# Optimization experiments

Hardware: AMD Instinct MI355X
Metric: run time of the kernel (lower is better)

## Reference

```python
import jax, jax.numpy as jnp
import numpy as np

N, H, T, E, L = 50000, 128, 4, 150000, 2
LAYER_TIMESTEPS = [3, 3]


def _gru_cell(x_in, h, Wih, Whh, bih, bhh):
    # PyTorch GRUCell semantics. Wih: [3H, in], Whh: [3H, H]
    gx = x_in @ Wih.T + bih
    gh = h @ Whh.T + bhh
    xr, xz, xn = jnp.split(gx, 3, axis=-1)
    hr, hz, hn = jnp.split(gh, 3, axis=-1)
    r = jax.nn.sigmoid(xr + hr)
    z = jax.nn.sigmoid(xz + hz)
    n = jnp.tanh(xn + r * hn)
    return (1.0 - z) * n + z * h


def setup_inputs() -> dict:
    key = jax.random.key(0)
    ks = jax.random.split(key, 16)
    s = 0.02
    inp = {
        'x': jax.random.normal(ks[0], (N, H), dtype=jnp.float32),
        'edges': jax.random.randint(ks[1], (T, E, 2), 0, N, dtype=jnp.int32),
        # per-layer, per-edge-type message linears (Linear: y = x W^T + b)
        'msg_W': jax.random.normal(ks[2], (L, T, H, H), dtype=jnp.float32) * s,
        'msg_b': jax.random.normal(ks[3], (L, T, H), dtype=jnp.float32) * s,
        # GRU layer 0: input dim H
        'gru0_Wih': jax.random.normal(ks[4], (3 * H, H), dtype=jnp.float32) * s,
        'gru0_Whh': jax.random.normal(ks[5], (3 * H, H), dtype=jnp.float32) * s,
        'gru0_bih': jax.random.normal(ks[6], (3 * H,), dtype=jnp.float32) * s,
        'gru0_bhh': jax.random.normal(ks[7], (3 * H,), dtype=jnp.float32) * s,
        # GRU layer 1: residual from layer 0 => input dim 2H
        'gru1_Wih': jax.random.normal(ks[8], (3 * H, 2 * H), dtype=jnp.float32) * s,
        'gru1_Whh': jax.random.normal(ks[9], (3 * H, H), dtype=jnp.float32) * s,
        'gru1_bih': jax.random.normal(ks[10], (3 * H,), dtype=jnp.float32) * s,
        'gru1_bhh': jax.random.normal(ks[11], (3 * H,), dtype=jnp.float32) * s,
    }
    return inp


def _incoming_messages(h, edges, W_l, b_l):
    # gather source states per edge type: [T, E, H]
    src = edges[:, :, 0]
    tgt = edges[:, :, 1]
    h_src = h[src]
    # per-edge-type linear: y = x W^T + b
    msgs = jnp.einsum('teh,tfh->tef', h_src, W_l) + b_l[:, None, :]
    # scatter-add messages onto target nodes (== dense one-hot matmul in original)
    return jax.ops.segment_sum(msgs.reshape(T * E, H), tgt.reshape(T * E), num_segments=N)


def reference(x, edges, msg_W, msg_b, gru0_Wih, gru0_Whh, gru0_bih, gru0_bhh,
              gru1_Wih, gru1_Whh, gru1_bih, gru1_bhh):
    # layer 0
    h = x
    for _ in range(LAYER_TIMESTEPS[0]):
        inc = _incoming_messages(h, edges, msg_W[0], msg_b[0])
        h = _gru_cell(inc, h, gru0_Wih, gru0_Whh, gru0_bih, gru0_bhh)
    h0_out = h
    # layer 1 with residual from initial node representation (layer index 0)
    h = h0_out
    for _ in range(LAYER_TIMESTEPS[1]):
        inc = _incoming_messages(h, edges, msg_W[1], msg_b[1])
        inp = jnp.concatenate([x, inc], axis=-1)  # residual states come first
        h = _gru_cell(inp, h, gru1_Wih, gru1_Whh, gru1_bih, gru1_bhh)
    return h
```

## Files before the change

kernel.cpp:

```cpp
#include <hip/hip_runtime.h>
#include <cstddef>

#define NN 50000
#define HH 128
#define TT 4
#define EE 150000

typedef __attribute__((ext_vector_type(8))) short bfrag8;
typedef __attribute__((ext_vector_type(4))) float f32x4;
typedef __attribute__((ext_vector_type(8))) unsigned short u16x8;

__device__ __forceinline__ float sigm(float v) { return 1.0f / (1.0f + __expf(-v)); }

__device__ __forceinline__ unsigned short f2b(float f) {
    unsigned int u = __float_as_uint(f);
    u += 0x7fffu + ((u >> 16) & 1u);
    return (unsigned short)(u >> 16);
}
__device__ __forceinline__ float b2f(unsigned short s) {
    return __uint_as_float(((unsigned int)s) << 16);
}

__device__ __forceinline__ void gload_lds16(const void* gp, void* lp) {
    __builtin_amdgcn_global_load_lds(
        (const __attribute__((address_space(1))) unsigned int*)gp,
        (__attribute__((address_space(3))) unsigned int*)lp, 16, 0, 0);
}

__device__ __forceinline__ void stage_w(const unsigned short* __restrict__ W, int K,
                                        int rowoff, int g8, unsigned short* ldsbase,
                                        int tid, int w, int lane) {
    #pragma unroll
    for (int i = 0; i < 2; ++i) {
        const int r = i * 64 + w * 8 + (lane >> 3);
        const int sc = g8 * 8 + ((lane & 7) ^ (r & 7));
        gload_lds16(W + (size_t)(rowoff + r) * K + sc * 8, ldsbase + (i * 512 + tid) * 8);
    }
}

__global__ __launch_bounds__(256)
void place_bucket(const int* __restrict__ edges, int* __restrict__ degT,
                  unsigned short* __restrict__ rowsT) {
    int eg = blockIdx.x * 256 + threadIdx.x;
    if (eg >= TT * EE) return;
    int t = eg / EE;
    int src = edges[eg * 2];
    int tgt = edges[eg * 2 + 1];
    int p = atomicAdd(&degT[t * NN + tgt], 1);
    if (p < 32) rowsT[((size_t)t * NN + tgt) * 32 + p] = (unsigned short)src;
}

__global__ __launch_bounds__(256)
void setup_convert(const float* __restrict__ msg_W,
                   const float* __restrict__ W0ih, const float* __restrict__ W0hh,
                   const float* __restrict__ W1ih, const float* __restrict__ W1hh,
                   const float* __restrict__ b0ih, const float* __restrict__ b0hh,
                   const float* __restrict__ b1ih, const float* __restrict__ b1hh,
                   const float* __restrict__ x, const int* __restrict__ degT,
                   unsigned int* __restrict__ degP,
                   unsigned short* __restrict__ wb, float* __restrict__ biasP,
                   unsigned short* __restrict__ xb, unsigned short* __restrict__ hbA,
                   unsigned short* __restrict__ hbB, float* __restrict__ out) {
    int i = blockIdx.x * 256 + threadIdx.x;
    if (i < NN) {
        unsigned int v0 = degT[i];            if (v0 > 32) v0 = 32;
        unsigned int v1 = degT[NN + i];       if (v1 > 32) v1 = 32;
        unsigned int v2 = degT[2 * NN + i];   if (v2 > 32) v2 = 32;
        unsigned int v3 = degT[3 * NN + i];   if (v3 > 32) v3 = 32;
        degP[i] = v0 | (v1 << 8) | (v2 << 16) | (v3 << 24);
        return;
    }
    i -= NN;
    if (i < 131072) {
        int l = i >> 16, r = i & 65535;
        int f = r >> 9, k = r & 511, t = k >> 7, h = k & 127;
        wb[i] = f2b(msg_W[l * 65536 + t * 16384 + f * 128 + h]);
        return;
    }
    i -= 131072;
    if (i < 65536) {
        int p = i >> 8, k = i & 255;
        int g = p >> 7, gc = p & 127;
        int f = g * 128 + gc;
        float v = (k < 128) ? W0ih[f * 128 + k] : W0hh[f * 128 + (k - 128)];
        wb[131072 + i] = f2b(v);
        return;
    }
    i -= 65536;
    if (i < 98304) {
        int p = i / 384, k = i - p * 384;
        int g = p >> 7, gc = p & 127;
        int f = g * 128 + gc;
        float v = (k < 256) ? W1ih[f * 256 + k] : W1hh[f * 128 + (k - 256)];
        wb[196608 + i] = f2b(v);
        return;
    }
    i -= 98304;
    if (i < 16384) {
        int gc = i >> 7, k = i & 127;
        wb[294912 + i] = f2b(W0ih[(256 + gc) * 128 + k]);
        return;
    }
    i -= 16384;
    if (i < 32768) {
        int gc = i >> 8, k = i & 255;
        wb[311296 + i] = f2b(W1ih[(256 + gc) * 256 + k]);
        return;
    }
    i -= 32768;
    if (i < 16384) {
        int gc = i >> 7, k = i & 127;
        wb[344064 + i] = f2b(W0hh[(256 + gc) * 128 + k]);
        return;
    }
    i -= 16384;
    if (i < 16384) {
        int gc = i >> 7, k = i & 127;
        wb[360448 + i] = f2b(W1hh[(256 + gc) * 128 + k]);
        return;
    }
    i -= 16384;
    if (i < 1024) {
        int l = i >> 9, r = i & 511;
        const float* bi = l ? b1ih : b0ih;
        const float* bh = l ? b1hh : b0hh;
        float v;
        if (r < 256) {
            int g = r >> 7, gc = r & 127;
            v = bi[g * 128 + gc] + bh[g * 128 + gc];
        } else if (r < 384) {
            v = bi[256 + (r - 256)];
        } else {
            v = bh[256 + (r - 384)];
        }
        biasP[i] = v;
        return;
    }
    i -= 1024;
    if (i < NN * HH) {
        float v = x[i];
        unsigned short b = f2b(v);
        xb[i] = b;
        hbA[i] = b;
        out[i] = v;
        return;
    }
    i -= NN * HH;
    if (i < 128) {
        hbA[(size_t)NN * 128 + i] = 0;
        hbB[(size_t)NN * 128 + i] = 0;
    }
}

template<int L>
__global__ __launch_bounds__(512, 4)
void step_kernel(const unsigned int* __restrict__ degP,
                 const unsigned short* __restrict__ rowsT,
                 const unsigned short* __restrict__ hb,
                 const unsigned short* __restrict__ xb,
                 const unsigned short* __restrict__ Bm,
                 const float* __restrict__ mb,
                 const unsigned short* __restrict__ Wrz,
                 const unsigned short* __restrict__ Wxn,
                 const unsigned short* __restrict__ Whn,
                 const float* __restrict__ bias,
                 const float* __restrict__ hcur,
                 float* __restrict__ hnext,
                 unsigned short* __restrict__ hbn) {
    constexpr int Kih = L ? 256 : 128;
    constexpr int KRZ = Kih + 128;
    constexpr int NRZ = KRZ / 64;
    constexpr int NXN = Kih / 64;
    constexpr int NT  = 2 * NRZ + NXN + 2;
    __shared__ unsigned short lds[32768];
    constexpr int OFF_S = 0, OFF_BMA = 16384, OFF_BMB = 24576;
    constexpr int OFF_X = 0;
    constexpr int OFF_I = L ? 8192 : 0;
    constexpr int OFF_H = L ? 16384 : 8192;
    constexpr int OFF_WA = L ? 24576 : 16384;
    constexpr int OFF_WB = 24576;

    const int tid = threadIdx.x;
    const int lane = tid & 63;
    const int w = tid >> 6;
    const int ln15 = lane & 15;
    const int quad = lane >> 4;
    const int swz = ln15 & 7;
    const int mbase = blockIdx.x * 64;

    auto do_gather = [&](int ta) {
        const int tsub = lane >> 5;
        const int t = ta + tsub;
        const int jh = (lane >> 4) & 1;
        const int cl = lane & 15;
        const int cc = cl * 8;
        int node0 = mbase + w * 8 + jh * 4;
        if (node0 > NN - 4) node0 = NN - 4;
        const uint4 dp4 = *(const uint4*)&degP[node0];
        const int tsh = t * 8;
        const size_t rbase = ((size_t)t * NN + node0) * 32;
        const u16x8 ix0 = *(const u16x8*)&rowsT[rbase];
        const u16x8 ix1 = *(const u16x8*)&rowsT[rbase + 32];
        const u16x8 ix2 = *(const u16x8*)&rowsT[rbase + 64];
        const u16x8 ix3 = *(const u16x8*)&rowsT[rbase + 96];
        #pragma unroll
        for (int jj = 0; jj < 4; ++jj) {
            const unsigned int dpw = (jj == 0) ? dp4.x : (jj == 1) ? dp4.y : (jj == 2) ? dp4.z : dp4.w;
            const int m = (int)((dpw >> tsh) & 255u);
            const u16x8 ix = (jj == 0) ? ix0 : (jj == 1) ? ix1 : (jj == 2) ? ix2 : ix3;
            float a[8] = {0.f, 0.f, 0.f, 0.f, 0.f, 0.f, 0.f, 0.f};
            #pragma unroll
            for (int q = 0; q < 8; ++q) {
                unsigned int rowi = (unsigned short)ix[q];
                if (q >= m) rowi = NN;
                const u16x8 v = *(const u16x8*)&hb[(size_t)rowi * 128 + cc];
                #pragma unroll
                for (int e = 0; e < 8; ++e) a[e] += b2f((unsigned short)v[e]);
            }
            if (m > 8) {
                const unsigned short* rp = &rowsT[rbase + jj * 32];
                for (int p = 8; p < m; ++p) {
                    const u16x8 v = *(const u16x8*)&hb[(size_t)rp[p] * 128 + cc];
                    #pragma unroll
                    for (int e = 0; e < 8; ++e) a[e] += b2f((unsigned short)v[e]);
                }
            }
            const int lrow = w * 8 + jh * 4 + jj;
            const int kg = tsub * 16 + cl;
            const int pos = (kg & ~7) | ((kg & 7) ^ (lrow & 7));
            u16x8 o;
            #pragma unroll
            for (int e = 0; e < 8; ++e) o[e] = f2b(a[e]);
            *(u16x8*)&lds[OFF_S + lrow * 256 + pos * 8] = o;
        }
    };

    f32x4 ainc[4];
    #pragma unroll
    for (int mt = 0; mt < 4; ++mt) ainc[mt] = (f32x4){0.f, 0.f, 0.f, 0.f};

    stage_w(Bm, 512, 0, 0, &lds[OFF_BMA], tid, w, lane);
    #pragma unroll
    for (int P = 0; P < 2; ++P) {
        do_gather(P * 2);
        __syncthreads();
        #pragma unroll
        for (int tt2 = 0; tt2 < 4; ++tt2) {
            const int tix = P * 4 + tt2;
            if (tix < 7)
                stage_w(Bm, 512, 0, tix + 1,
                        &lds[((tix + 1) & 1) ? OFF_BMB : OFF_BMA], tid, w, lane);
            const int bmoff = (tix & 1) ? OFF_BMB : OFF_BMA;
            #pragma unroll
            for (int kk = 0; kk < 2; ++kk) {
                const int cpos = (kk * 4 + quad) ^ swz;
                bfrag8 aFv[4];
                #pragma unroll
                for (int mt = 0; mt < 4; ++mt)
                    aFv[mt] = *(const bfrag8*)&lds[OFF_S + (mt * 16 + ln15) * 256 + (tt2 * 8 + cpos) * 8];
                const bfrag8 bFv = *(const bfrag8*)&lds[bmoff + ((w * 16 + ln15) * 8 + cpos) * 8];
                #pragma unroll
                for (int mt = 0; mt < 4; ++mt)
                    ainc[mt] = __builtin_amdgcn_mfma_f32_16x16x32_bf16(aFv[mt], bFv, ainc[mt], 0, 0, 0);
            }
            __syncthreads();
        }
    }

    #pragma unroll
    for (int i = 0; i < 2; ++i) {
        const int r0 = i * 32 + w * 4;
        const int row = r0 + (lane >> 4);
        const int pos = lane & 15;
        int grow = mbase + row;
        if (grow > NN - 1) grow = NN - 1;
        const int sc = (pos & 8) | ((pos & 7) ^ (row & 7));
        const size_t off = (size_t)grow * 128 + sc * 8;
        if (L == 1) gload_lds16(xb + off, &lds[OFF_X + r0 * 128]);
        gload_lds16(hb + off, &lds[OFF_H + r0 * 128]);
    }
    stage_w(Wrz, KRZ, 0, 0, &lds[OFF_WA], tid, w, lane);
    {
        const int gc = w * 16 + ln15;
        const float bt0 = mb[gc], bt1 = mb[128 + gc], bt2 = mb[256 + gc], bt3 = mb[384 + gc];
        const int chunk = gc >> 3;
        const int sub = gc & 7;
        #pragma unroll
        for (int mt = 0; mt < 4; ++mt) {
            #pragma unroll
            for (int reg = 0; reg < 4; ++reg) {
                const int lrow = mt * 16 + quad * 4 + reg;
                int row = mbase + lrow;
                if (row > NN - 1) row = NN - 1;
                const unsigned int dp = degP[row];
                const float v = ainc[mt][reg]
                    + (float)(dp & 255u) * bt0 + (float)((dp >> 8) & 255u) * bt1
                    + (float)((dp >> 16) & 255u) * bt2 + (float)((dp >> 24) & 255u) * bt3;
                const int pos = (chunk & 8) | ((chunk & 7) ^ (lrow & 7));
                lds[OFF_I + lrow * 128 + pos * 8 + sub] = f2b(v);
            }
        }
    }
    __syncthreads();

    f32x4 arz0[4], arz1[4], axn[4], ahn[4];
    #pragma unroll
    for (int mt = 0; mt < 4; ++mt) {
        arz0[mt] = (f32x4){0.f, 0.f, 0.f, 0.f};
        arz1[mt] = (f32x4){0.f, 0.f, 0.f, 0.f};
        axn[mt] = (f32x4){0.f, 0.f, 0.f, 0.f};
        ahn[mt] = (f32x4){0.f, 0.f, 0.f, 0.f};
    }

    auto stage_T = [&](int T, int woff) {
        if (L == 0) {
            if (T < 8)       stage_w(Wrz, KRZ, (T >> 2) * 128, T & 3, &lds[woff], tid, w, lane);
            else if (T < 10) stage_w(Wxn, Kih, 0, T - 8, &lds[woff], tid, w, lane);
            else             stage_w(Whn, 128, 0, T - 10, &lds[woff], tid, w, lane);
        } else {
            if (T < 12)      stage_w(Wrz, KRZ, (T / 6) * 128, T % 6, &lds[woff], tid, w, lane);
            else if (T < 16) stage_w(Wxn, Kih, 0, T - 12, &lds[woff], tid, w, lane);
            else             stage_w(Whn, 128, 0, T - 16, &lds[woff], tid, w, lane);
        }
    };
    auto mfma_T = [&](int T, int woff) {
        int abase, ha;
        f32x4* acc;
        if (L == 0) {
            if (T < 8)       { const int hh = T & 3; abase = hh < 2 ? OFF_I : OFF_H; ha = hh & 1; acc = (T >> 2) ? arz1 : arz0; }
            else if (T < 10) { abase = OFF_I; ha = T - 8; acc = axn; }
            else             { abase = OFF_H; ha = T - 10; acc = ahn; }
        } else {
            if (T < 12)      { const int hh = T % 6; abase = hh < 2 ? OFF_X : (hh < 4 ? OFF_I : OFF_H); ha = hh & 1; acc = (T / 6) ? arz1 : arz0; }
            else if (T < 16) { const int hh = T - 12; abase = hh < 2 ? OFF_X : OFF_I; ha = hh & 1; acc = axn; }
            else             { abase = OFF_H; ha = T - 16; acc = ahn; }
        }
        #pragma unroll
        for (int kk = 0; kk < 2; ++kk) {
            const int cpos = (kk * 4 + quad) ^ swz;
            bfrag8 aFv[4];
            #pragma unroll
            for (int mt = 0; mt < 4; ++mt)
                aFv[mt] = *(const bfrag8*)&lds[abase + (mt * 16 + ln15) * 128 + (ha * 8 + cpos) * 8];
            const bfrag8 bFv = *(const bfrag8*)&lds[woff + ((w * 16 + ln15) * 8 + cpos) * 8];
            #pragma unroll
            for (int mt = 0; mt < 4; ++mt)
                acc[mt] = __builtin_amdgcn_mfma_f32_16x16x32_bf16(aFv[mt], bFv, acc[mt], 0, 0, 0);
        }
    };

    if (L == 0) {
        #pragma unroll
        for (int T = 0; T < NT; ++T) {
            if (T + 1 < NT) stage_T(T + 1, ((T + 1) & 1) ? OFF_WB : OFF_WA);
            mfma_T(T, (T & 1) ? OFF_WB : OFF_WA);
            __syncthreads();
        }
    } else {
        #pragma unroll
        for (int T = 0; T < NT; ++T) {
            mfma_T(T, OFF_WB);
            if (T + 1 < NT) {
                __syncthreads();
                stage_T(T + 1, OFF_WB);
                __syncthreads();
            }
        }
    }

    {
        const int gc = w * 16 + ln15;
        const float br = bias[gc];
        const float bz = bias[128 + gc];
        const float bxnv = bias[256 + gc];
        const float bhnv = bias[384 + gc];
        #pragma unroll
        for (int mt = 0; mt < 4; ++mt) {
            #pragma unroll
            for (int reg = 0; reg < 4; ++reg) {
                const int row = mbase + mt * 16 + quad * 4 + reg;
                if (row < NN) {
                    const float r = sigm(arz0[mt][reg] + br);
                    const float z = sigm(arz1[mt][reg] + bz);
                    const float n = tanhf(axn[mt][reg] + bxnv + r * (ahn[mt][reg] + bhnv));
                    const float h = hcur[(size_t)row * 128 + gc];
                    const float o = (1.f - z) * n + z * h;
                    hnext[(size_t)row * 128 + gc] = o;
                    if (hbn) hbn[(size_t)row * 128 + gc] = f2b(o);
                }
            }
        }
    }
}

extern "C" void kernel_launch(void* const* d_in, const int* in_sizes, int n_in,
                              void* d_out, int out_size, void* d_ws, size_t ws_size,
                              hipStream_t stream) {
    (void)in_sizes; (void)n_in; (void)out_size; (void)ws_size;
    const float* x     = (const float*)d_in[0];
    const int*   edges = (const int*)d_in[1];
    const float* msg_W = (const float*)d_in[2];
    const float* msg_b = (const float*)d_in[3];
    const float* W0ih  = (const float*)d_in[4];
    const float* W0hh  = (const float*)d_in[5];
    const float* b0ih  = (const float*)d_in[6];
    const float* b0hh  = (const float*)d_in[7];
    const float* W1ih  = (const float*)d_in[8];
    const float* W1hh  = (const float*)d_in[9];
    const float* b1ih  = (const float*)d_in[10];
    const float* b1hh  = (const float*)d_in[11];
    float* out = (float*)d_out;

    float* ws = (float*)d_ws;
    unsigned short* xb  = (unsigned short*)ws;
    unsigned short* hbA = (unsigned short*)(ws + 3200000);
    unsigned short* hbB = (unsigned short*)(ws + 6400100);
    float* hA           = ws + 9700000;
    unsigned short* wb  = (unsigned short*)(ws + 16200000);
    float* biasP        = ws + 16400000;
    int* degT           = (int*)(ws + 16500000);
    unsigned int* degP  = (unsigned int*)(ws + 16750000);
    unsigned short* rowsT = (unsigned short*)(ws + 16850000);

    unsigned short* Bmsg = wb;
    unsigned short* Wrz0 = wb + 131072;
    unsigned short* Wrz1 = wb + 196608;
    unsigned short* Wxn0 = wb + 294912;
    unsigned short* Wxn1 = wb + 311296;
    unsigned short* Whn0 = wb + 344064;
    unsigned short* Whn1 = wb + 360448;

    hipMemsetAsync(degT, 0, (size_t)NN * 4 * sizeof(int), stream);
    place_bucket<<<(TT * EE + 255) / 256, 256, 0, stream>>>(edges, degT, rowsT);

    setup_convert<<<26672, 256, 0, stream>>>(msg_W, W0ih, W0hh, W1ih, W1hh,
                                             b0ih, b0hh, b1ih, b1hh, x,
                                             degT, degP, wb, biasP, xb, hbA, hbB, out);

    const int gblocks = (NN + 63) / 64;
    for (int s = 0; s < 6; ++s) {
        const int l = s / 3;
        const float* hcur  = (s % 2 == 0) ? out : hA;
        float*       hnext = (s % 2 == 0) ? hA : out;
        unsigned short* hbc = (s % 2 == 0) ? hbA : hbB;
        unsigned short* hbn = (s % 2 == 0) ? hbB : hbA;
        if (s == 5) hbn = nullptr;
        if (l == 0)
            step_kernel<0><<<gblocks, 512, 0, stream>>>(
                degP, rowsT, hbc, xb, Bmsg, msg_b, Wrz0, Wxn0, Whn0,
                biasP, hcur, hnext, hbn);
        else
            step_kernel<1><<<gblocks, 512, 0, stream>>>(
                degP, rowsT, hbc, xb, Bmsg + 65536, msg_b + 512, Wrz1, Wxn1, Whn1,
                biasP + 512, hcur, hnext, hbn);
    }
}
```

Measured before the change: 617.2 us.

## Split step into gather and gate kernels with fragment-ordered weights read from global

Weights are pre-permuted at setup into MFMA B-fragment order, so each lane loads its bf16x8 fragment straight from global/L2 instead of staging weight tiles through LDS with barriers. The fused step kernel is split into a gather+message kernel that writes a bf16 incoming-message buffer, and a GRU gate kernel that loads that buffer into LDS. This removes many LDS staging syncs and shrinks LDS use for higher occupancy, at the cost of an extra global round trip for the message tensor and an extra launch per step.

```diff
diff --git a/kernel.cpp b/kernel.cpp
--- a/kernel.cpp
+++ b/kernel.cpp
@@ -25,17 +25,6 @@
     __builtin_amdgcn_global_load_lds(
         (const __attribute__((address_space(1))) unsigned int*)gp,
         (__attribute__((address_space(3))) unsigned int*)lp, 16, 0, 0);
-}
-
-__device__ __forceinline__ void stage_w(const unsigned short* __restrict__ W, int K,
-                                        int rowoff, int g8, unsigned short* ldsbase,
-                                        int tid, int w, int lane) {
-    #pragma unroll
-    for (int i = 0; i < 2; ++i) {
-        const int r = i * 64 + w * 8 + (lane >> 3);
-        const int sc = g8 * 8 + ((lane & 7) ^ (r & 7));
-        gload_lds16(W + (size_t)(rowoff + r) * K + sc * 8, ldsbase + (i * 512 + tid) * 8);
-    }
 }
 
 __global__ __launch_bounds__(256)
@@ -73,49 +62,67 @@
     i -= NN;
     if (i < 131072) {
         int l = i >> 16, r = i & 65535;
-        int f = r >> 9, k = r & 511, t = k >> 7, h = k & 127;
+        int e = r & 7, lane = (r >> 3) & 63, kc = (r >> 9) & 15, ocg = (r >> 13) & 7;
+        int f = ocg * 16 + (lane & 15);
+        int k = kc * 32 + (lane >> 4) * 8 + e;
+        int t = k >> 7, h = k & 127;
         wb[i] = f2b(msg_W[l * 65536 + t * 16384 + f * 128 + h]);
         return;
     }
     i -= 131072;
     if (i < 65536) {
-        int p = i >> 8, k = i & 255;
+        int e = i & 7, lane = (i >> 3) & 63, kc = (i >> 9) & 7, ocg = (i >> 12) & 15;
+        int p = ocg * 16 + (lane & 15);
         int g = p >> 7, gc = p & 127;
-        int f = g * 128 + gc;
-        float v = (k < 128) ? W0ih[f * 128 + k] : W0hh[f * 128 + (k - 128)];
+        int k = kc * 32 + (lane >> 4) * 8 + e;
+        float v = (k < 128) ? W0ih[(g * 128 + gc) * 128 + k] : W0hh[(g * 128 + gc) * 128 + (k - 128)];
         wb[131072 + i] = f2b(v);
         return;
     }
     i -= 65536;
     if (i < 98304) {
-        int p = i / 384, k = i - p * 384;
+        int e = i & 7, lane = (i >> 3) & 63, rem = i >> 9;
+        int kc = rem % 12, ocg = rem / 12;
+        int p = ocg * 16 + (lane & 15);
         int g = p >> 7, gc = p & 127;
-        int f = g * 128 + gc;
-        float v = (k < 256) ? W1ih[f * 256 + k] : W1hh[f * 128 + (k - 256)];
+        int k = kc * 32 + (lane >> 4) * 8 + e;
+        float v = (k < 256) ? W1ih[(g * 128 + gc) * 256 + k] : W1hh[(g * 128 + gc) * 128 + (k - 256)];
         wb[196608 + i] = f2b(v);
         return;
     }
     i -= 98304;
     if (i < 16384) {
-        int gc = i >> 7, k = i & 127;
+        int e = i & 7, lane = (i >> 3) & 63, rem = i >> 9;
+        int kc = rem & 3, ocg = rem >> 2;
+        int gc = ocg * 16 + (lane & 15);
+        int k = kc * 32 + (lane >> 4) * 8 + e;
         wb[294912 + i] = f2b(W0ih[(256 + gc) * 128 + k]);
         return;
     }
     i -= 16384;
     if (i < 32768) {
-        int gc = i >> 8, k = i & 255;
+        int e = i & 7, lane = (i >> 3) & 63;
+        int kc = (i >> 9) & 7, ocg = (i >> 12) & 7;
+        int gc = ocg * 16 + (lane & 15);
+        int k = kc * 32 + (lane >> 4) * 8 + e;
         wb[311296 + i] = f2b(W1ih[(256 + gc) * 256 + k]);
         return;
     }
     i -= 32768;
     if (i < 16384) {
-        int gc = i >> 7, k = i & 127;
+        int e = i & 7, lane = (i >> 3) & 63, rem = i >> 9;
+        int kc = rem & 3, ocg = rem >> 2;
+        int gc = ocg * 16 + (lane & 15);
+        int k = kc * 32 + (lane >> 4) * 8 + e;
         wb[344064 + i] = f2b(W0hh[(256 + gc) * 128 + k]);
         return;
     }
     i -= 16384;
     if (i < 16384) {
-        int gc = i >> 7, k = i & 127;
+        int e = i & 7, lane = (i >> 3) & 63, rem = i >> 9;
+        int kc = rem & 3, ocg = rem >> 2;
+        int gc = ocg * 16 + (lane & 15);
+        int k = kc * 32 + (lane >> 4) * 8 + e;
         wb[360448 + i] = f2b(W1hh[(256 + gc) * 128 + k]);
         return;
     }
@@ -152,33 +159,14 @@
     }
 }
 
-template<int L>
-__global__ __launch_bounds__(512, 4)
-void step_kernel(const unsigned int* __restrict__ degP,
-                 const unsigned short* __restrict__ rowsT,
-                 const unsigned short* __restrict__ hb,
-                 const unsigned short* __restrict__ xb,
-                 const unsigned short* __restrict__ Bm,
-                 const float* __restrict__ mb,
-                 const unsigned short* __restrict__ Wrz,
-                 const unsigned short* __restrict__ Wxn,
-                 const unsigned short* __restrict__ Whn,
-                 const float* __restrict__ bias,
-                 const float* __restrict__ hcur,
-                 float* __restrict__ hnext,
-                 unsigned short* __restrict__ hbn) {
-    constexpr int Kih = L ? 256 : 128;
-    constexpr int KRZ = Kih + 128;
-    constexpr int NRZ = KRZ / 64;
-    constexpr int NXN = Kih / 64;
-    constexpr int NT  = 2 * NRZ + NXN + 2;
-    __shared__ unsigned short lds[32768];
-    constexpr int OFF_S = 0, OFF_BMA = 16384, OFF_BMB = 24576;
-    constexpr int OFF_X = 0;
-    constexpr int OFF_I = L ? 8192 : 0;
-    constexpr int OFF_H = L ? 16384 : 8192;
-    constexpr int OFF_WA = L ? 24576 : 16384;
-    constexpr int OFF_WB = 24576;
+__global__ __launch_bounds__(512, 6)
+void gather_inc(const unsigned int* __restrict__ degP,
+                const unsigned short* __restrict__ rowsT,
+                const unsigned short* __restrict__ hb,
+                const unsigned short* __restrict__ BmFL,
+                const float* __restrict__ mb,
+                unsigned short* __restrict__ incb) {
+    __shared__ unsigned short lds[16384];
 
     const int tid = threadIdx.x;
     const int lane = tid & 63;
@@ -231,7 +219,7 @@
             u16x8 o;
             #pragma unroll
             for (int e = 0; e < 8; ++e) o[e] = f2b(a[e]);
-            *(u16x8*)&lds[OFF_S + lrow * 256 + pos * 8] = o;
+            *(u16x8*)&lds[lrow * 256 + pos * 8] = o;
         }
     };
 
@@ -239,33 +227,68 @@
     #pragma unroll
     for (int mt = 0; mt < 4; ++mt) ainc[mt] = (f32x4){0.f, 0.f, 0.f, 0.f};
 
-    stage_w(Bm, 512, 0, 0, &lds[OFF_BMA], tid, w, lane);
     #pragma unroll
     for (int P = 0; P < 2; ++P) {
         do_gather(P * 2);
         __syncthreads();
         #pragma unroll
-        for (int tt2 = 0; tt2 < 4; ++tt2) {
-            const int tix = P * 4 + tt2;
-            if (tix < 7)
-                stage_w(Bm, 512, 0, tix + 1,
-                        &lds[((tix + 1) & 1) ? OFF_BMB : OFF_BMA], tid, w, lane);
-            const int bmoff = (tix & 1) ? OFF_BMB : OFF_BMA;
+        for (int j = 0; j < 8; ++j) {
+            const bfrag8 bF = *(const bfrag8*)&BmFL[(size_t)((w * 16 + P * 8 + j) * 64 + lane) * 8];
+            const int c = j * 4 + quad;
+            const int pos = (c & ~7) | ((c & 7) ^ swz);
             #pragma unroll
-            for (int kk = 0; kk < 2; ++kk) {
-                const int cpos = (kk * 4 + quad) ^ swz;
-                bfrag8 aFv[4];
-                #pragma unroll
-                for (int mt = 0; mt < 4; ++mt)
-                    aFv[mt] = *(const bfrag8*)&lds[OFF_S + (mt * 16 + ln15) * 256 + (tt2 * 8 + cpos) * 8];
-                const bfrag8 bFv = *(const bfrag8*)&lds[bmoff + ((w * 16 + ln15) * 8 + cpos) * 8];
-                #pragma unroll
-                for (int mt = 0; mt < 4; ++mt)
-                    ainc[mt] = __builtin_amdgcn_mfma_f32_16x16x32_bf16(aFv[mt], bFv, ainc[mt], 0, 0, 0);
+            for (int mt = 0; mt < 4; ++mt) {
+                const bfrag8 aF = *(const bfrag8*)&lds[(mt * 16 + ln15) * 256 + pos * 8];
+                ainc[mt] = __builtin_amdgcn_mfma_f32_16x16x32_bf16(aF, bF, ainc[mt], 0, 0, 0);
             }
-            __syncthreads();
-        }
-    }
+        }
+        if (P == 0) __syncthreads();
+    }
+
+    const int gc = w * 16 + ln15;
+    const float bt0 = mb[gc], bt1 = mb[128 + gc], bt2 = mb[256 + gc], bt3 = mb[384 + gc];
+    #pragma unroll
+    for (int mt = 0; mt < 4; ++mt) {
+        #pragma unroll
+        for (int reg = 0; reg < 4; ++reg) {
+            const int row = mbase + mt * 16 + quad * 4 + reg;
+            if (row < NN) {
+                const unsigned int dp = degP[row];
+                const float v = ainc[mt][reg]
+                    + (float)(dp & 255u) * bt0 + (float)((dp >> 8) & 255u) * bt1
+                    + (float)((dp >> 16) & 255u) * bt2 + (float)((dp >> 24) & 255u) * bt3;
+                incb[(size_t)row * 128 + gc] = f2b(v);
+            }
+        }
+    }
+}
+
+template<int L>
+__global__ __launch_bounds__(512, 4)
+void gate_kernel(const unsigned short* __restrict__ incb,
+                 const unsigned short* __restrict__ xb,
+                 const unsigned short* __restrict__ hb,
+                 const unsigned short* __restrict__ WrzFL,
+                 const unsigned short* __restrict__ WxnFL,
+                 const unsigned short* __restrict__ WhnFL,
+                 const float* __restrict__ bias,
+                 const float* __restrict__ hcur,
+                 float* __restrict__ hnext,
+                 unsigned short* __restrict__ hbn) {
+    constexpr int KCrz = L ? 12 : 8;
+    constexpr int KCxn = L ? 8 : 4;
+    __shared__ unsigned short lds[L ? 24576 : 16384];
+    constexpr int OFF_X = 0;
+    constexpr int OFF_I = L ? 8192 : 0;
+    constexpr int OFF_H = L ? 16384 : 8192;
+
+    const int tid = threadIdx.x;
+    const int lane = tid & 63;
+    const int w = tid >> 6;
+    const int ln15 = lane & 15;
+    const int quad = lane >> 4;
+    const int swz = ln15 & 7;
+    const int mbase = blockIdx.x * 64;
 
     #pragma unroll
     for (int i = 0; i < 2; ++i) {
@@ -277,117 +300,80 @@
         const int sc = (pos & 8) | ((pos & 7) ^ (row & 7));
         const size_t off = (size_t)grow * 128 + sc * 8;
         if (L == 1) gload_lds16(xb + off, &lds[OFF_X + r0 * 128]);
+        gload_lds16(incb + off, &lds[OFF_I + r0 * 128]);
         gload_lds16(hb + off, &lds[OFF_H + r0 * 128]);
     }
-    stage_w(Wrz, KRZ, 0, 0, &lds[OFF_WA], tid, w, lane);
-    {
-        const int gc = w * 16 + ln15;
-        const float bt0 = mb[gc], bt1 = mb[128 + gc], bt2 = mb[256 + gc], bt3 = mb[384 + gc];
-        const int chunk = gc >> 3;
-        const int sub = gc & 7;
+    __syncthreads();
+
+    f32x4 ar[4], az[4], ax[4], ah[4];
+    #pragma unroll
+    for (int mt = 0; mt < 4; ++mt) {
+        ar[mt] = (f32x4){0.f, 0.f, 0.f, 0.f};
+        az[mt] = (f32x4){0.f, 0.f, 0.f, 0.f};
+        ax[mt] = (f32x4){0.f, 0.f, 0.f, 0.f};
+        ah[mt] = (f32x4){0.f, 0.f, 0.f, 0.f};
+    }
+
+    #pragma unroll
+    for (int kc = 0; kc < KCrz; ++kc) {
+        const int abase = (L == 1) ? (kc < 4 ? OFF_X : (kc < 8 ? OFF_I : OFF_H))
+                                   : (kc < 4 ? OFF_I : OFF_H);
+        const int c = (kc & 3) * 4 + quad;
+        const int pos = (c & 8) | ((c & 7) ^ swz);
+        bfrag8 aF[4];
+        #pragma unroll
+        for (int mt = 0; mt < 4; ++mt)
+            aF[mt] = *(const bfrag8*)&lds[abase + (mt * 16 + ln15) * 128 + pos * 8];
+        const bfrag8 bR = *(const bfrag8*)&WrzFL[(size_t)((w * KCrz + kc) * 64 + lane) * 8];
+        const bfrag8 bZ = *(const bfrag8*)&WrzFL[(size_t)(((w + 8) * KCrz + kc) * 64 + lane) * 8];
         #pragma unroll
         for (int mt = 0; mt < 4; ++mt) {
-            #pragma unroll
-            for (int reg = 0; reg < 4; ++reg) {
-                const int lrow = mt * 16 + quad * 4 + reg;
-                int row = mbase + lrow;
-                if (row > NN - 1) row = NN - 1;
-                const unsigned int dp = degP[row];
-                const float v = ainc[mt][reg]
-                    + (float)(dp & 255u) * bt0 + (float)((dp >> 8) & 255u) * bt1
-                    + (float)((dp >> 16) & 255u) * bt2 + (float)((dp >> 24) & 255u) * bt3;
-                const int pos = (chunk & 8) | ((chunk & 7) ^ (lrow & 7));
-                lds[OFF_I + lrow * 128 + pos * 8 + sub] = f2b(v);
-            }
-        }
-    }
-    __syncthreads();
-
-    f32x4 arz0[4], arz1[4], axn[4], ahn[4];
+            ar[mt] = __builtin_amdgcn_mfma_f32_16x16x32_bf16(aF[mt], bR, ar[mt], 0, 0, 0);
+            az[mt] = __builtin_amdgcn_mfma_f32_16x16x32_bf16(aF[mt], bZ, az[mt], 0, 0, 0);
+        }
+    }
+    #pragma unroll
+    for (int kc = 0; kc < KCxn; ++kc) {
+        const int abase = (L == 1) ? (kc < 4 ? OFF_X : OFF_I) : OFF_I;
+        const int c = (kc & 3) * 4 + quad;
+        const int pos = (c & 8) | ((c & 7) ^ swz);
+        const bfrag8 bX = *(const bfrag8*)&WxnFL[(size_t)((w * KCxn + kc) * 64 + lane) * 8];
+        #pragma unroll
+        for (int mt = 0; mt < 4; ++mt) {
+            const bfrag8 aF = *(const bfrag8*)&lds[abase + (mt * 16 + ln15) * 128 + pos * 8];
+            ax[mt] = __builtin_amdgcn_mfma_f32_16x16x32_bf16(aF, bX, ax[mt], 0, 0, 0);
+        }
+    }
+    #pragma unroll
+    for (int kc = 0; kc < 4; ++kc) {
+        const int c = kc * 4 + quad;
+        const int pos = (c & 8) | ((c & 7) ^ swz);
+        const bfrag8 bH = *(const bfrag8*)&WhnFL[(size_t)((w * 4 + kc) * 64 + lane) * 8];
+        #pragma unroll
+        for (int mt = 0; mt < 4; ++mt) {
+            const bfrag8 aF = *(const bfrag8*)&lds[OFF_H + (mt * 16 + ln15) * 128 + pos * 8];
+            ah[mt] = __builtin_amdgcn_mfma_f32_16x16x32_bf16(aF, bH, ah[mt], 0, 0, 0);
+        }
+    }
+
+    const int gc = w * 16 + ln15;
+    const float br = bias[gc];
+    const float bz = bias[128 + gc];
+    const float bxnv = bias[256 + gc];
+    const float bhnv = bias[384 + gc];
     #pragma unroll
     for (int mt = 0; mt < 4; ++mt) {
-        arz0[mt] = (f32x4){0.f, 0.f, 0.f, 0.f};
-        arz1[mt] = (f32x4){0.f, 0.f, 0.f, 0.f};
-        axn[mt] = (f32x4){0.f, 0.f, 0.f, 0.f};
-        ahn[mt] = (f32x4){0.f, 0.f, 0.f, 0.f};
-    }
-
-    auto stage_T = [&](int T, int woff) {
-        if (L == 0) {
-            if (T < 8)       stage_w(Wrz, KRZ, (T >> 2) * 128, T & 3, &lds[woff], tid, w, lane);
-            else if (T < 10) stage_w(Wxn, Kih, 0, T - 8, &lds[woff], tid, w, lane);
-            else             stage_w(Whn, 128, 0, T - 10, &lds[woff], tid, w, lane);
-        } else {
-            if (T < 12)      stage_w(Wrz, KRZ, (T / 6) * 128, T % 6, &lds[woff], tid, w, lane);
-            else if (T < 16) stage_w(Wxn, Kih, 0, T - 12, &lds[woff], tid, w, lane);
-            else             stage_w(Whn, 128, 0, T - 16, &lds[woff], tid, w, lane);
-        }
-    };
-    auto mfma_T = [&](int T, int woff) {
-        int abase, ha;
-        f32x4* acc;
-        if (L == 0) {
-            if (T < 8)       { const int hh = T & 3; abase = hh < 2 ? OFF_I : OFF_H; ha = hh & 1; acc = (T >> 2) ? arz1 : arz0; }
-            else if (T < 10) { abase = OFF_I; ha = T - 8; acc = axn; }
-            else             { abase = OFF_H; ha = T - 10; acc = ahn; }
-        } else {
-            if (T < 12)      { const int hh = T % 6; abase = hh < 2 ? OFF_X : (hh < 4 ? OFF_I : OFF_H); ha = hh & 1; acc = (T / 6) ? arz1 : arz0; }
-            else if (T < 16) { const int hh = T - 12; abase = hh < 2 ? OFF_X : OFF_I; ha = hh & 1; acc = axn; }
-            else             { abase = OFF_H; ha = T - 16; acc = ahn; }
-        }
-        #pragma unroll
-        for (int kk = 0; kk < 2; ++kk) {
-            const int cpos = (kk * 4 + quad) ^ swz;
-            bfrag8 aFv[4];
-            #pragma unroll
-            for (int mt = 0; mt < 4; ++mt)
-                aFv[mt] = *(const bfrag8*)&lds[abase + (mt * 16 + ln15) * 128 + (ha * 8 + cpos) * 8];
-            const bfrag8 bFv = *(const bfrag8*)&lds[woff + ((w * 16 + ln15) * 8 + cpos) * 8];
-            #pragma unroll
-            for (int mt = 0; mt < 4; ++mt)
-                acc[mt] = __builtin_amdgcn_mfma_f32_16x16x32_bf16(aFv[mt], bFv, acc[mt], 0, 0, 0);
-        }
-    };
-
-    if (L == 0) {
-        #pragma unroll
-        for (int T = 0; T < NT; ++T) {
-            if (T + 1 < NT) stage_T(T + 1, ((T + 1) & 1) ? OFF_WB : OFF_WA);
-            mfma_T(T, (T & 1) ? OFF_WB : OFF_WA);
-            __syncthreads();
-        }
-    } else {
-        #pragma unroll
-        for (int T = 0; T < NT; ++T) {
-            mfma_T(T, OFF_WB);
-            if (T + 1 < NT) {
-                __syncthreads();
-                stage_T(T + 1, OFF_WB);
-                __syncthreads();
-            }
-        }
-    }
-
-    {
-        const int gc = w * 16 + ln15;
-        const float br = bias[gc];
-        const float bz = bias[128 + gc];
-        const float bxnv = bias[256 + gc];
-        const float bhnv = bias[384 + gc];
-        #pragma unroll
-        for (int mt = 0; mt < 4; ++mt) {
-            #pragma unroll
-            for (int reg = 0; reg < 4; ++reg) {
-                const int row = mbase + mt * 16 + quad * 4 + reg;
-                if (row < NN) {
-                    const float r = sigm(arz0[mt][reg] + br);
-                    const float z = sigm(arz1[mt][reg] + bz);
-                    const float n = tanhf(axn[mt][reg] + bxnv + r * (ahn[mt][reg] + bhnv));
-                    const float h = hcur[(size_t)row * 128 + gc];
-                    const float o = (1.f - z) * n + z * h;
-                    hnext[(size_t)row * 128 + gc] = o;
-                    if (hbn) hbn[(size_t)row * 128 + gc] = f2b(o);
-                }
+        #pragma unroll
+        for (int reg = 0; reg < 4; ++reg) {
+            const int row = mbase + mt * 16 + quad * 4 + reg;
+            if (row < NN) {
+                const float r = sigm(ar[mt][reg] + br);
+                const float z = sigm(az[mt][reg] + bz);
+                const float n = tanhf(ax[mt][reg] + bxnv + r * (ah[mt][reg] + bhnv));
+                const float h = hcur[(size_t)row * 128 + gc];
+                const float o = (1.f - z) * n + z * h;
+                hnext[(size_t)row * 128 + gc] = o;
+                if (hbn) hbn[(size_t)row * 128 + gc] = f2b(o);
             }
         }
     }
@@ -421,14 +407,15 @@
     int* degT           = (int*)(ws + 16500000);
     unsigned int* degP  = (unsigned int*)(ws + 16750000);
     unsigned short* rowsT = (unsigned short*)(ws + 16850000);
-
-    unsigned short* Bmsg = wb;
-    unsigned short* Wrz0 = wb + 131072;
-    unsigned short* Wrz1 = wb + 196608;
-    unsigned short* Wxn0 = wb + 294912;
-    unsigned short* Wxn1 = wb + 311296;
-    unsigned short* Whn0 = wb + 344064;
-    unsigned short* Whn1 = wb + 360448;
+    unsigned short* incb  = (unsigned short*)(ws + 20100000);
+
+    unsigned short* BmFL   = wb;
+    unsigned short* WrzFL0 = wb + 131072;
+    unsigned short* WrzFL1 = wb + 196608;
+    unsigned short* WxnFL0 = wb + 294912;
+    unsigned short* WxnFL1 = wb + 311296;
+    unsigned short* WhnFL0 = wb + 344064;
+    unsigned short* WhnFL1 = wb + 360448;
 
     hipMemsetAsync(degT, 0, (size_t)NN * 4 * sizeof(int), stream);
     place_bucket<<<(TT * EE + 255) / 256, 256, 0, stream>>>(edges, degT, rowsT);
@@ -445,13 +432,16 @@
         unsigned short* hbc = (s % 2 == 0) ? hbA : hbB;
         unsigned short* hbn = (s % 2 == 0) ? hbB : hbA;
         if (s == 5) hbn = nullptr;
+
+        gather_inc<<<gblocks, 512, 0, stream>>>(
+            degP, rowsT, hbc, BmFL + (size_t)l * 65536, msg_b + (size_t)l * 512, incb);
         if (l == 0)
-            step_kernel<0><<<gblocks, 512, 0, stream>>>(
-                degP, rowsT, hbc, xb, Bmsg, msg_b, Wrz0, Wxn0, Whn0,
-                biasP, hcur, hnext, hbn);
+            gate_kernel<0><<<gblocks, 512, 0, stream>>>(
+                incb, xb, hbc, WrzFL0, WxnFL0, WhnFL0, biasP,
+                hcur, hnext, hbn);
         else
-            step_kernel<1><<<gblocks, 512, 0, stream>>>(
-                degP, rowsT, hbc, xb, Bmsg + 65536, msg_b + 512, Wrz1, Wxn1, Whn1,
-                biasP + 512, hcur, hnext, hbn);
-    }
-}
+            gate_kernel<1><<<gblocks, 512, 0, stream>>>(
+                incb, xb, hbc, WrzFL1, WxnFL1, WhnFL1, biasP + 512,
+                hcur, hnext, hbn);
+    }
+}
```

Measured after the change: 705.7 us. 14.3% more time.
